# Optimization experiments

Measured on AMD Instinct MI355X. Metric: run time of the kernel, lower is better.

## Reference

```python
import jax, jax.numpy as jnp
import numpy as np
import math

L, B, S, D, H, F, C = 2, 2, 1024, 512, 32, 2048, 1000
EPS_LN = 1e-5

def _grid_coords(batch, seq_len):
    g = math.ceil(math.sqrt(seq_len))
    xs = jnp.linspace(0.0, 1.0, g)
    gx, gy = jnp.meshgrid(xs, xs, indexing='ij')
    pts = jnp.stack([gx.ravel(), gy.ravel()], axis=1)
    reps = math.ceil(seq_len / (g * g))
    pts = jnp.tile(pts, (reps, 1))[:seq_len]
    return jnp.broadcast_to(pts[None], (batch, seq_len, 2)).astype(jnp.float32)

def setup_inputs() -> dict:
    key = jax.random.key(0)
    ks = iter(jax.random.split(key, 16))
    sd = 0.02
    inp = {
        'x': jax.random.normal(next(ks), (B, S, D), jnp.float32),
        'coords': _grid_coords(B, S),
        'Wq': jax.random.normal(next(ks), (L, D, D), jnp.float32) * sd,
        'Wk': jax.random.normal(next(ks), (L, D, D), jnp.float32) * sd,
        'Wv': jax.random.normal(next(ks), (L, D, D), jnp.float32) * sd,
        'rot_w1': jax.random.normal(next(ks), (L, 3, H), jnp.float32) * 0.5,
        'rot_b1': jnp.zeros((L, H), jnp.float32),
        'rot_w2': jax.random.normal(next(ks), (L, H), jnp.float32) * 0.1,
        'rot_b2': jnp.zeros((L,), jnp.float32),
        'trans_w1': jax.random.normal(next(ks), (L, 2, H), jnp.float32) * 0.5,
        'trans_b1': jnp.zeros((L, H), jnp.float32),
        'trans_w2': jax.random.normal(next(ks), (L, H), jnp.float32) * 0.1,
        'trans_b2': jnp.zeros((L,), jnp.float32),
        'refl_w1': jax.random.normal(next(ks), (L, 4, H), jnp.float32) * 0.5,
        'refl_b1': jnp.zeros((L, H), jnp.float32),
        'refl_w2': jax.random.normal(next(ks), (L, H), jnp.float32) * 0.1,
        'refl_b2': jnp.zeros((L,), jnp.float32),
        'ln1_g': jnp.ones((L, D), jnp.float32),
        'ln1_b': jnp.zeros((L, D), jnp.float32),
        'ffn_w1': jax.random.normal(next(ks), (L, D, F), jnp.float32) * sd,
        'ffn_b1': jnp.zeros((L, F), jnp.float32),
        'ffn_w2': jax.random.normal(next(ks), (L, F, D), jnp.float32) * sd,
        'ffn_b2': jnp.zeros((L, D), jnp.float32),
        'ln2_g': jnp.ones((L, D), jnp.float32),
        'ln2_b': jnp.zeros((L, D), jnp.float32),
        'lnf_g': jnp.ones((D,), jnp.float32),
        'lnf_b': jnp.zeros((D,), jnp.float32),
        'fc_w': jax.random.normal(next(ks), (D, C), jnp.float32) * sd,
        'fc_b': jnp.zeros((C,), jnp.float32),
    }
    return inp

def _layernorm(x, g, b):
    mu = x.mean(-1, keepdims=True)
    var = ((x - mu) ** 2).mean(-1, keepdims=True)
    return (x - mu) * jax.lax.rsqrt(var + EPS_LN) * g + b

def _pair_mlp(inp, w1, b1, w2, b2):
    # inp: [B,S,S,f] -> [B,S,S]
    h = jax.nn.relu(jnp.einsum('bijf,fh->bijh', inp, w1) + b1)
    return jnp.einsum('bijh,h->bij', h, w2) + b2

def reference(x, coords, Wq, Wk, Wv, rot_w1, rot_b1, rot_w2, rot_b2,
              trans_w1, trans_b1, trans_w2, trans_b2,
              refl_w1, refl_b1, refl_w2, refl_b2,
              ln1_g, ln1_b, ffn_w1, ffn_b1, ffn_w2, ffn_b2, ln2_g, ln2_b,
              lnf_g, lnf_b, fc_w, fc_b):
    d_model = x.shape[-1]
    scale = math.sqrt(d_model)
    # Pairwise relative geometry (layer-independent): rel = coords_j - coords_i
    rel = coords[:, None, :, :] - coords[:, :, None, :]   # [B,S,S,2]
    dx, dy = rel[..., 0], rel[..., 1]
    dist = jnp.sqrt(dx * dx + dy * dy + 1e-8)
    theta = jnp.arctan2(dy, dx)
    rot_in = jnp.stack([dist, jnp.sin(theta), jnp.cos(theta)], axis=-1)  # [B,S,S,3]
    trans_in = rel                                                       # [B,S,S,2]
    refl_in = jnp.concatenate([rel, -rel], axis=-1)                      # [B,S,S,4]

    n_layers = Wq.shape[0]
    for l in range(n_layers):
        Q = x @ Wq[l]
        K = x @ Wk[l]
        V = x @ Wv[l]
        scores = jnp.einsum('bid,bjd->bij', Q, K) / scale
        scores = scores \
            + _pair_mlp(rot_in, rot_w1[l], rot_b1[l], rot_w2[l], rot_b2[l]) \
            + _pair_mlp(trans_in, trans_w1[l], trans_b1[l], trans_w2[l], trans_b2[l]) \
            + _pair_mlp(refl_in, refl_w1[l], refl_b1[l], refl_w2[l], refl_b2[l])
        attn = jax.nn.softmax(scores, axis=-1)
        attn_out = jnp.einsum('bij,bjd->bid', attn, V)
        x = _layernorm(x + attn_out, ln1_g[l], ln1_b[l])
        ffn = jax.nn.relu(x @ ffn_w1[l] + ffn_b1[l]) @ ffn_w2[l] + ffn_b2[l]
        x = _layernorm(x + ffn, ln2_g[l], ln2_b[l])

    x = _layernorm(x, lnf_g, lnf_b)
    pooled = x.mean(axis=1)          # [B,D]
    return pooled @ fc_w + fc_b      # [B,C]
```

## Files before the change

### kernel.cpp

```cpp
#include <hip/hip_runtime.h>
#include <hip/hip_bf16.h>

using bf16 = __hip_bfloat16;
typedef __attribute__((ext_vector_type(8))) short short8;
typedef __attribute__((ext_vector_type(4))) float f32x4;

constexpr int NLAYER = 2;
constexpr int NB = 2;
constexpr int NS = 1024;
constexpr int ND = 512;
constexpr int NH = 32;
constexpr int NF = 2048;
constexpr int NC = 1000;
constexpr float EPS_LN = 1e-5f;

__device__ inline unsigned short f2bfu(float x) {
    union { bf16 h; unsigned short u; } c;
    c.h = __float2bfloat16(x);
    return c.u;
}

#define GLOAD16(gp, lp) __builtin_amdgcn_global_load_lds( \
    (const __attribute__((address_space(1))) void*)(gp),  \
    (__attribute__((address_space(3))) void*)(lp), 16, 0, 0)

template<int BM, int BN, bool OUTBF, bool RELU, bool SCORES, bool VOUT>
__global__ __launch_bounds__(256) void mfma_gemm(
    const bf16* __restrict__ A, const bf16* __restrict__ B,
    const float* __restrict__ bias, void* __restrict__ Cout,
    const float* __restrict__ table, bf16* __restrict__ vT,
    int K, int lda, int ldb, int ldc,
    long sA, long sB, long sC, float alpha)
{
    const int bz = blockIdx.z;
    A += (long)bz * sA;
    B += (long)bz * sB;
    const int bm = blockIdx.y * BM, bn = blockIdx.x * BN;
    __shared__ bf16 As[2][BM * 32], Bs[2][BN * 32];
    const int tid = threadIdx.x, lane = tid & 63, wv = tid >> 6;
    const int wr = (wv >> 1) * (BM / 2), wc = (wv & 1) * (BN / 2);
    constexpr int FM = BM / 32, FN = BN / 32;
    f32x4 acc[FM][FN] = {};
    const int r_a = tid >> 2;
    const int ko = (tid & 3) * 8;

    auto stage = [&](int buf, int k0) {
        #pragma unroll
        for (int c = 0; c < BM / 64; ++c)
            GLOAD16(A + (long)(bm + r_a + c * 64) * lda + k0 + ko,
                    &As[buf][c * 2048 + wv * 512]);
        #pragma unroll
        for (int c = 0; c < BN / 64; ++c)
            GLOAD16(B + (long)(bn + r_a + c * 64) * ldb + k0 + ko,
                    &Bs[buf][c * 2048 + wv * 512]);
    };

    const int nt = K >> 5;
    stage(0, 0);
    __syncthreads();
    for (int t = 0; t < nt; ++t) {
        const int cur = t & 1;
        if (t + 1 < nt) stage(cur ^ 1, (t + 1) << 5);
        const short8* Asv = (const short8*)As[cur];
        const short8* Bsv = (const short8*)Bs[cur];
        short8 af[FM], bfr[FN];
        #pragma unroll
        for (int m = 0; m < FM; ++m)
            af[m] = Asv[(wr + m * 16 + (lane & 15)) * 4 + (lane >> 4)];
        #pragma unroll
        for (int n = 0; n < FN; ++n)
            bfr[n] = Bsv[(wc + n * 16 + (lane & 15)) * 4 + (lane >> 4)];
        #pragma unroll
        for (int m = 0; m < FM; ++m)
            #pragma unroll
            for (int n = 0; n < FN; ++n)
                acc[m][n] = __builtin_amdgcn_mfma_f32_16x16x32_bf16(
                    af[m], bfr[n], acc[m][n], 0, 0, 0);
        __syncthreads();
    }

    const int er = (lane >> 4) * 4, ec = lane & 15;
    #pragma unroll
    for (int m = 0; m < FM; ++m) {
        #pragma unroll
        for (int n = 0; n < FN; ++n) {
            const int row0 = bm + wr + m * 16 + er;
            const int col  = bn + wc + n * 16 + ec;
            const float bv = bias ? bias[col] : 0.f;
            #pragma unroll
            for (int e = 0; e < 4; ++e) {
                const int row = row0 + e;
                float v = acc[m][n][e];
                if (SCORES) {
                    int di = (col >> 5) - (row >> 5) + 31;
                    int dj = (col & 31) - (row & 31) + 31;
                    v = v * alpha + table[di * 63 + dj];
                } else {
                    v += bv;
                    if (RELU) v = fmaxf(v, 0.f);
                }
                if (OUTBF)
                    ((bf16*)Cout)[bz * sC + (long)row * ldc + col] = __float2bfloat16(v);
                else
                    ((float*)Cout)[bz * sC + (long)row * ldc + col] = v;
                if (VOUT && col >= 2 * ND) {
                    int bb = row >> 10;
                    vT[(long)bb * ND * NS + (long)(col - 2 * ND) * NS + (row & (NS - 1))] =
                        __float2bfloat16(v);
                }
            }
        }
    }
}

__global__ __launch_bounds__(256) void tconv_qkv_kernel(
    const float* __restrict__ Wq, const float* __restrict__ Wk,
    const float* __restrict__ Wv, bf16* __restrict__ dst)
{
    const int z = blockIdx.z;
    const int l = z / 3, wsel = z % 3;
    const float* src = (wsel == 0 ? Wq : wsel == 1 ? Wk : Wv) + (long)l * ND * ND;
    bf16* d = dst + (long)l * 3 * ND * ND + (long)wsel * ND * ND;
    __shared__ float t[32][33];
    const int c0 = blockIdx.x * 32, r0 = blockIdx.y * 32;
    const int lx = threadIdx.x & 31, ly = threadIdx.x >> 5;
    for (int rr = ly; rr < 32; rr += 8)
        t[rr][lx] = src[(long)(r0 + rr) * ND + c0 + lx];
    __syncthreads();
    for (int cc = ly; cc < 32; cc += 8)
        d[(long)(c0 + cc) * ND + r0 + lx] = __float2bfloat16(t[lx][cc]);
}

__global__ __launch_bounds__(256) void tconv_f32_kernel(
    const float* __restrict__ src, bf16* __restrict__ dst,
    int R, int C, long sS, long sD)
{
    src += (long)blockIdx.z * sS;
    dst += (long)blockIdx.z * sD;
    __shared__ float t[32][33];
    const int c0 = blockIdx.x * 32, r0 = blockIdx.y * 32;
    const int lx = threadIdx.x & 31, ly = threadIdx.x >> 5;
    for (int rr = ly; rr < 32; rr += 8)
        t[rr][lx] = src[(long)(r0 + rr) * C + c0 + lx];
    __syncthreads();
    for (int cc = ly; cc < 32; cc += 8)
        dst[(long)(c0 + cc) * R + r0 + lx] = __float2bfloat16(t[lx][cc]);
}

__global__ __launch_bounds__(256) void xcopy_kernel(
    const float* __restrict__ xin, float* __restrict__ xc, bf16* __restrict__ xb)
{
    long i = (long)blockIdx.x * 256 + threadIdx.x;
    float4 v = ((const float4*)xin)[i];
    ((float4*)xc)[i] = v;
    uint2 o;
    o.x = (unsigned)f2bfu(v.x) | ((unsigned)f2bfu(v.y) << 16);
    o.y = (unsigned)f2bfu(v.z) | ((unsigned)f2bfu(v.w) << 16);
    ((uint2*)xb)[i] = o;
}

__global__ __launch_bounds__(256) void bias_table_kernel(
    const float* __restrict__ coords,
    const float* __restrict__ rot_w1, const float* __restrict__ rot_b1,
    const float* __restrict__ rot_w2, const float* __restrict__ rot_b2,
    const float* __restrict__ trans_w1, const float* __restrict__ trans_b1,
    const float* __restrict__ trans_w2, const float* __restrict__ trans_b2,
    const float* __restrict__ refl_w1, const float* __restrict__ refl_b1,
    const float* __restrict__ refl_w2, const float* __restrict__ refl_b2,
    float* __restrict__ table)
{
    int idx = blockIdx.x * 256 + threadIdx.x;
    if (idx >= 63 * 63) return;
    int da = idx / 63 - 31, db = idx % 63 - 31;
    int ai = da < 0 ? -da : 0, bi = db < 0 ? -db : 0;
    int i = ai * 32 + bi, j = (ai + da) * 32 + (bi + db);
    float2 ci = ((const float2*)coords)[i];
    float2 cj = ((const float2*)coords)[j];
    float dx = cj.x - ci.x, dy = cj.y - ci.y;
    float dist = sqrtf(dx * dx + dy * dy + 1e-8f);
    float th = atan2f(dy, dx);
    float sn = sinf(th), cs = cosf(th);

    #pragma unroll
    for (int l = 0; l < NLAYER; ++l) {
        const float* rw1 = rot_w1 + l * 3 * NH;
        const float* rb1 = rot_b1 + l * NH;
        const float* rw2 = rot_w2 + l * NH;
        const float* tw1 = trans_w1 + l * 2 * NH;
        const float* tb1 = trans_b1 + l * NH;
        const float* tw2 = trans_w2 + l * NH;
        const float* fw1 = refl_w1 + l * 4 * NH;
        const float* fb1 = refl_b1 + l * NH;
        const float* fw2 = refl_w2 + l * NH;
        float acc = rot_b2[l] + trans_b2[l] + refl_b2[l];
        #pragma unroll 8
        for (int h = 0; h < NH; ++h) {
            float hr = fmaxf(dist * rw1[h] + sn * rw1[NH + h] + cs * rw1[2 * NH + h] + rb1[h], 0.f);
            acc += hr * rw2[h];
            float ht = fmaxf(dx * tw1[h] + dy * tw1[NH + h] + tb1[h], 0.f);
            acc += ht * tw2[h];
            float hf = fmaxf(dx * fw1[h] + dy * fw1[NH + h] - dx * fw1[2 * NH + h] - dy * fw1[3 * NH + h] + fb1[h], 0.f);
            acc += hf * fw2[h];
        }
        table[l * 3969 + idx] = acc;
    }
}

__global__ __launch_bounds__(256) void init_tail_kernel(
    const float* __restrict__ fc_b, float* __restrict__ out, float* __restrict__ pooled)
{
    int i = blockIdx.x * 256 + threadIdx.x;
    if (i < NB * NC) out[i] = fc_b[i % NC];
    int j = i - NB * NC;
    if (j >= 0 && j < NB * ND) pooled[j] = 0.f;
}

__global__ __launch_bounds__(256) void softmax_kernel(
    const float* __restrict__ sc, bf16* __restrict__ P)
{
    const float* p = sc + (long)blockIdx.x * NS;
    const int tid = threadIdx.x;
    float4 v = ((const float4*)p)[tid];
    float m = fmaxf(fmaxf(v.x, v.y), fmaxf(v.z, v.w));
    #pragma unroll
    for (int off = 32; off; off >>= 1) m = fmaxf(m, __shfl_xor(m, off));
    __shared__ float red[4], red2[4];
    int wid = tid >> 6;
    if ((tid & 63) == 0) red[wid] = m;
    __syncthreads();
    m = fmaxf(fmaxf(red[0], red[1]), fmaxf(red[2], red[3]));
    v.x = __expf(v.x - m); v.y = __expf(v.y - m);
    v.z = __expf(v.z - m); v.w = __expf(v.w - m);
    float s = v.x + v.y + v.z + v.w;
    #pragma unroll
    for (int off = 32; off; off >>= 1) s += __shfl_xor(s, off);
    if ((tid & 63) == 0) red2[wid] = s;
    __syncthreads();
    s = red2[0] + red2[1] + red2[2] + red2[3];
    float inv = 1.f / s;
    uint2 o;
    o.x = (unsigned)f2bfu(v.x * inv) | ((unsigned)f2bfu(v.y * inv) << 16);
    o.y = (unsigned)f2bfu(v.z * inv) | ((unsigned)f2bfu(v.w * inv) << 16);
    ((uint2*)(P + (long)blockIdx.x * NS))[tid] = o;
}

__global__ __launch_bounds__(256) void add_ln_kernel(
    const float* __restrict__ x, const float* __restrict__ res,
    const float* __restrict__ g, const float* __restrict__ bt,
    float* __restrict__ out, bf16* __restrict__ outb)
{
    long row = blockIdx.x;
    const int tid = threadIdx.x;
    float2 xv = ((const float2*)(x + row * ND))[tid];
    if (res) {
        float2 rv = ((const float2*)(res + row * ND))[tid];
        xv.x += rv.x; xv.y += rv.y;
    }
    float s = xv.x + xv.y;
    float ss = xv.x * xv.x + xv.y * xv.y;
    #pragma unroll
    for (int off = 32; off; off >>= 1) {
        s += __shfl_xor(s, off);
        ss += __shfl_xor(ss, off);
    }
    __shared__ float rs[4], rss[4];
    int wid = tid >> 6;
    if ((tid & 63) == 0) { rs[wid] = s; rss[wid] = ss; }
    __syncthreads();
    s = rs[0] + rs[1] + rs[2] + rs[3];
    ss = rss[0] + rss[1] + rss[2] + rss[3];
    float mu = s * (1.f / ND);
    float var = ss * (1.f / ND) - mu * mu;
    float inv = rsqrtf(var + EPS_LN);
    float2 gv = ((const float2*)g)[tid];
    float2 bv = ((const float2*)bt)[tid];
    float2 o;
    o.x = (xv.x - mu) * inv * gv.x + bv.x;
    o.y = (xv.y - mu) * inv * gv.y + bv.y;
    ((float2*)(out + row * ND))[tid] = o;
    if (outb)
        ((unsigned int*)(outb + row * ND))[tid] =
            (unsigned)f2bfu(o.x) | ((unsigned)f2bfu(o.y) << 16);
}

__global__ __launch_bounds__(256) void pool_kernel(
    const float* __restrict__ x, float* __restrict__ pooled)
{
    const int tid = threadIdx.x;
    const long row0 = (long)blockIdx.x * 16;
    const int b = (int)(row0 >> 10);
    float ax = 0.f, ay = 0.f, az = 0.f, aw = 0.f;
    #pragma unroll
    for (int it = 0; it < 8; ++it) {
        long r = row0 + it * 2 + (tid >> 7);
        float4 v = ((const float4*)(x + r * ND))[tid & 127];
        ax += v.x; ay += v.y; az += v.z; aw += v.w;
    }
    __shared__ float red[256][4];
    red[tid][0] = ax; red[tid][1] = ay; red[tid][2] = az; red[tid][3] = aw;
    __syncthreads();
    if (tid < 128) {
        int d = tid * 4;
        atomicAdd(&pooled[b * ND + d + 0], (red[tid][0] + red[tid + 128][0]) * (1.f / NS));
        atomicAdd(&pooled[b * ND + d + 1], (red[tid][1] + red[tid + 128][1]) * (1.f / NS));
        atomicAdd(&pooled[b * ND + d + 2], (red[tid][2] + red[tid + 128][2]) * (1.f / NS));
        atomicAdd(&pooled[b * ND + d + 3], (red[tid][3] + red[tid + 128][3]) * (1.f / NS));
    }
}

__global__ __launch_bounds__(256) void fc_kernel(
    const float* __restrict__ pooled, const float* __restrict__ w,
    float* __restrict__ out)
{
    const int lane = threadIdx.x & 63, dg = threadIdx.x >> 6;
    const int c = blockIdx.x * 64 + lane;
    const int b = blockIdx.y;
    const int d0 = blockIdx.z * 64 + dg * 16;
    const bool ok = (c < NC);
    const float* p = pooled + b * ND;
    float acc = 0.f;
    #pragma unroll
    for (int d = 0; d < 16; ++d)
        acc += p[d0 + d] * (ok ? w[(long)(d0 + d) * NC + c] : 0.f);
    __shared__ float red[4][64];
    red[dg][lane] = acc;
    __syncthreads();
    if (dg == 0 && ok)
        atomicAdd(&out[(long)b * NC + c],
                  red[0][lane] + red[1][lane] + red[2][lane] + red[3][lane]);
}

extern "C" void kernel_launch(void* const* d_in, const int* in_sizes, int n_in,
                              void* d_out, int out_size, void* d_ws, size_t ws_size,
                              hipStream_t stream)
{
    const float* x_in   = (const float*)d_in[0];
    const float* coords = (const float*)d_in[1];
    const float* Wq     = (const float*)d_in[2];
    const float* Wk     = (const float*)d_in[3];
    const float* Wv     = (const float*)d_in[4];
    const float* rot_w1 = (const float*)d_in[5];
    const float* rot_b1 = (const float*)d_in[6];
    const float* rot_w2 = (const float*)d_in[7];
    const float* rot_b2 = (const float*)d_in[8];
    const float* trans_w1 = (const float*)d_in[9];
    const float* trans_b1 = (const float*)d_in[10];
    const float* trans_w2 = (const float*)d_in[11];
    const float* trans_b2 = (const float*)d_in[12];
    const float* refl_w1 = (const float*)d_in[13];
    const float* refl_b1 = (const float*)d_in[14];
    const float* refl_w2 = (const float*)d_in[15];
    const float* refl_b2 = (const float*)d_in[16];
    const float* ln1_g = (const float*)d_in[17];
    const float* ln1_b = (const float*)d_in[18];
    const float* ffn_w1 = (const float*)d_in[19];
    const float* ffn_b1 = (const float*)d_in[20];
    const float* ffn_w2 = (const float*)d_in[21];
    const float* ffn_b2 = (const float*)d_in[22];
    const float* ln2_g = (const float*)d_in[23];
    const float* ln2_b = (const float*)d_in[24];
    const float* lnf_g = (const float*)d_in[25];
    const float* lnf_b = (const float*)d_in[26];
    const float* fc_w = (const float*)d_in[27];
    const float* fc_b = (const float*)d_in[28];
    float* out = (float*)d_out;

    const long XSZ = (long)NB * NS * ND;
    const long SSZ = (long)NB * NS * NS;

    char* wp = (char*)d_ws;
    auto alloc = [&](long bytes) -> char* {
        char* p = wp; wp += (bytes + 255) & ~(long)255; return p;
    };
    float* x_cur  = (float*)alloc(XSZ * 4);
    bf16*  xb     = (bf16*)alloc(XSZ * 2);
    bf16*  qkv    = (bf16*)alloc((long)NB * NS * 1536 * 2);
    bf16*  vT     = (bf16*)alloc((long)NB * ND * NS * 2);
    float* sc     = (float*)alloc(SSZ * 4);
    bf16*  pb     = (bf16*)alloc(SSZ * 2);
    float* ao     = (float*)alloc(XSZ * 4);
    bf16*  hfb    = (bf16*)alloc((long)NB * NS * NF * 2);
    bf16*  wqkvT  = (bf16*)alloc((long)NLAYER * 3 * ND * ND * 2);
    bf16*  w1T    = (bf16*)alloc((long)NLAYER * NF * ND * 2);
    bf16*  w2T    = (bf16*)alloc((long)NLAYER * ND * NF * 2);
    float* table  = (float*)alloc((long)NLAYER * 3969 * 4);
    float* pooled = (float*)alloc((long)NB * ND * 4);

    const float inv_scale = 1.0f / sqrtf((float)ND);
    const long QKVLD = 1536;

    tconv_qkv_kernel<<<dim3(16, 16, 3 * NLAYER), 256, 0, stream>>>(Wq, Wk, Wv, wqkvT);
    tconv_f32_kernel<<<dim3(64, 16, NLAYER), 256, 0, stream>>>(
        ffn_w1, w1T, ND, NF, (long)ND * NF, (long)NF * ND);
    tconv_f32_kernel<<<dim3(16, 64, NLAYER), 256, 0, stream>>>(
        ffn_w2, w2T, NF, ND, (long)NF * ND, (long)ND * NF);

    xcopy_kernel<<<dim3((int)(XSZ / 1024)), 256, 0, stream>>>(x_in, x_cur, xb);

    bias_table_kernel<<<dim3(16), 256, 0, stream>>>(
        coords, rot_w1, rot_b1, rot_w2, rot_b2,
        trans_w1, trans_b1, trans_w2, trans_b2,
        refl_w1, refl_b1, refl_w2, refl_b2, table);

    init_tail_kernel<<<dim3(12), 256, 0, stream>>>(fc_b, out, pooled);

    for (int l = 0; l < NLAYER; ++l) {
        mfma_gemm<128, 128, true, false, false, true>
            <<<dim3(1536 / 128, (NB * NS) / 128, 1), 256, 0, stream>>>(
            xb, wqkvT + (long)l * 3 * ND * ND, nullptr, qkv, nullptr, vT,
            ND, ND, ND, QKVLD, 0, 0, 0, 0.f);

        mfma_gemm<128, 128, false, false, true, false>
            <<<dim3(NS / 128, NS / 128, NB), 256, 0, stream>>>(
            qkv, qkv + ND, nullptr, sc, table + (long)l * 3969, nullptr,
            ND, QKVLD, QKVLD, NS, (long)NS * QKVLD, (long)NS * QKVLD,
            (long)NS * NS, inv_scale);

        softmax_kernel<<<dim3(NB * NS), 256, 0, stream>>>(sc, pb);

        mfma_gemm<128, 64, false, false, false, false>
            <<<dim3(ND / 64, NS / 128, NB), 256, 0, stream>>>(
            pb, vT, nullptr, ao, nullptr, nullptr,
            NS, NS, NS, ND, (long)NS * NS, (long)ND * NS, (long)NS * ND, 0.f);

        add_ln_kernel<<<dim3(NB * NS), 256, 0, stream>>>(
            x_cur, ao, ln1_g + (long)l * ND, ln1_b + (long)l * ND, x_cur, xb);

        mfma_gemm<128, 128, true, true, false, false>
            <<<dim3(NF / 128, (NB * NS) / 128, 1), 256, 0, stream>>>(
            xb, w1T + (long)l * NF * ND, ffn_b1 + (long)l * NF, hfb, nullptr, nullptr,
            ND, ND, ND, NF, 0, 0, 0, 0.f);

        mfma_gemm<128, 64, false, false, false, false>
            <<<dim3(ND / 64, (NB * NS) / 128, 1), 256, 0, stream>>>(
            hfb, w2T + (long)l * ND * NF, ffn_b2 + (long)l * ND, ao, nullptr, nullptr,
            NF, NF, NF, ND, 0, 0, 0, 0.f);

        add_ln_kernel<<<dim3(NB * NS), 256, 0, stream>>>(
            x_cur, ao, ln2_g + (long)l * ND, ln2_b + (long)l * ND, x_cur, xb);
    }

    add_ln_kernel<<<dim3(NB * NS), 256, 0, stream>>>(
        x_cur, nullptr, lnf_g, lnf_b, x_cur, nullptr);

    pool_kernel<<<dim3((NB * NS) / 16), 256, 0, stream>>>(x_cur, pooled);

    fc_kernel<<<dim3((NC + 63) / 64, NB, ND / 64), 256, 0, stream>>>(pooled, fc_w, out);
}
```

Measured before the change: 388.4 us.

## Use 8-wave GEMM blocks and merge setup kernels into fewer launches

The MFMA GEMM now runs with 512 threads (8 waves) and a configurable wave grid, so each wave computes a smaller sub-tile. The staging loop is rewritten to distribute 16-row chunks across waves. The PV and FFN2 GEMMs switch from 128x64 tiles to 64x128 tiles. The weight transposes are merged into one launch, and the x copy, bias table and output init into another, to cut launch overhead. The trade-off is fewer accumulator registers per wave for more waves per block. More threads can also share each LDS tile, which changes barrier cost.

Measured after the change: 384.3 us. About the same (-1.0%).

```diff
diff --git a/kernel.cpp b/kernel.cpp
--- a/kernel.cpp
+++ b/kernel.cpp
@@ -24,8 +24,8 @@
     (const __attribute__((address_space(1))) void*)(gp),  \
     (__attribute__((address_space(3))) void*)(lp), 16, 0, 0)
 
-template<int BM, int BN, bool OUTBF, bool RELU, bool SCORES, bool VOUT>
-__global__ __launch_bounds__(256) void mfma_gemm(
+template<int BM, int BN, int WR, int WC, bool OUTBF, bool RELU, bool SCORES, bool VOUT>
+__global__ __launch_bounds__(512) void mfma_gemm(
     const bf16* __restrict__ A, const bf16* __restrict__ B,
     const float* __restrict__ bias, void* __restrict__ Cout,
     const float* __restrict__ table, bf16* __restrict__ vT,
@@ -38,21 +38,26 @@
     const int bm = blockIdx.y * BM, bn = blockIdx.x * BN;
     __shared__ bf16 As[2][BM * 32], Bs[2][BN * 32];
     const int tid = threadIdx.x, lane = tid & 63, wv = tid >> 6;
-    const int wr = (wv >> 1) * (BM / 2), wc = (wv & 1) * (BN / 2);
-    constexpr int FM = BM / 32, FN = BN / 32;
+    constexpr int WM = BM / WR, WN = BN / WC;
+    constexpr int FM = WM / 16, FN = WN / 16;
+    const int wr = (wv / WC) * WM, wc = (wv % WC) * WN;
     f32x4 acc[FM][FN] = {};
-    const int r_a = tid >> 2;
-    const int ko = (tid & 3) * 8;
+    const int ko = (lane & 3) * 8;
+    constexpr int ACH = BM / 16;
+    constexpr int BCH = BN / 16;
+    constexpr int NCH = ACH + BCH;
 
     auto stage = [&](int buf, int k0) {
-        #pragma unroll
-        for (int c = 0; c < BM / 64; ++c)
-            GLOAD16(A + (long)(bm + r_a + c * 64) * lda + k0 + ko,
-                    &As[buf][c * 2048 + wv * 512]);
-        #pragma unroll
-        for (int c = 0; c < BN / 64; ++c)
-            GLOAD16(B + (long)(bn + r_a + c * 64) * ldb + k0 + ko,
-                    &Bs[buf][c * 2048 + wv * 512]);
+        for (int c = wv; c < NCH; c += 8) {
+            if (c < ACH) {
+                int r = c * 16 + (lane >> 2);
+                GLOAD16(A + (long)(bm + r) * lda + k0 + ko, &As[buf][c * 512]);
+            } else {
+                int cc = c - ACH;
+                int r = cc * 16 + (lane >> 2);
+                GLOAD16(B + (long)(bn + r) * ldb + k0 + ko, &Bs[buf][cc * 512]);
+            }
+        }
     };
 
     const int nt = K >> 5;
@@ -113,32 +118,32 @@
     }
 }
 
-__global__ __launch_bounds__(256) void tconv_qkv_kernel(
+__global__ __launch_bounds__(256) void wtrans_kernel(
     const float* __restrict__ Wq, const float* __restrict__ Wk,
-    const float* __restrict__ Wv, bf16* __restrict__ dst)
-{
-    const int z = blockIdx.z;
-    const int l = z / 3, wsel = z % 3;
-    const float* src = (wsel == 0 ? Wq : wsel == 1 ? Wk : Wv) + (long)l * ND * ND;
-    bf16* d = dst + (long)l * 3 * ND * ND + (long)wsel * ND * ND;
+    const float* __restrict__ Wv, const float* __restrict__ ffn_w1,
+    const float* __restrict__ ffn_w2, bf16* __restrict__ wqkvT,
+    bf16* __restrict__ w1T, bf16* __restrict__ w2T)
+{
+    const int s = blockIdx.x;
+    const float* src; bf16* dst; int R, C, r0, c0;
+    if (s < 1536) {
+        int z = s >> 8, rem = s & 255;
+        int l = z / 3, wsel = z % 3;
+        src = (wsel == 0 ? Wq : wsel == 1 ? Wk : Wv) + (long)l * ND * ND;
+        dst = wqkvT + (long)l * 3 * ND * ND + (long)wsel * ND * ND;
+        R = ND; C = ND; c0 = (rem & 15) * 32; r0 = (rem >> 4) * 32;
+    } else if (s < 3584) {
+        int t = s - 1536, l = t >> 10, rem = t & 1023;
+        src = ffn_w1 + (long)l * ND * NF;
+        dst = w1T + (long)l * NF * ND;
+        R = ND; C = NF; c0 = (rem & 63) * 32; r0 = (rem >> 6) * 32;
+    } else {
+        int t = s - 3584, l = t >> 10, rem = t & 1023;
+        src = ffn_w2 + (long)l * NF * ND;
+        dst = w2T + (long)l * ND * NF;
+        R = NF; C = ND; c0 = (rem & 15) * 32; r0 = (rem >> 4) * 32;
+    }
     __shared__ float t[32][33];
-    const int c0 = blockIdx.x * 32, r0 = blockIdx.y * 32;
-    const int lx = threadIdx.x & 31, ly = threadIdx.x >> 5;
-    for (int rr = ly; rr < 32; rr += 8)
-        t[rr][lx] = src[(long)(r0 + rr) * ND + c0 + lx];
-    __syncthreads();
-    for (int cc = ly; cc < 32; cc += 8)
-        d[(long)(c0 + cc) * ND + r0 + lx] = __float2bfloat16(t[lx][cc]);
-}
-
-__global__ __launch_bounds__(256) void tconv_f32_kernel(
-    const float* __restrict__ src, bf16* __restrict__ dst,
-    int R, int C, long sS, long sD)
-{
-    src += (long)blockIdx.z * sS;
-    dst += (long)blockIdx.z * sD;
-    __shared__ float t[32][33];
-    const int c0 = blockIdx.x * 32, r0 = blockIdx.y * 32;
     const int lx = threadIdx.x & 31, ly = threadIdx.x >> 5;
     for (int rr = ly; rr < 32; rr += 8)
         t[rr][lx] = src[(long)(r0 + rr) * C + c0 + lx];
@@ -147,19 +152,8 @@
         dst[(long)(c0 + cc) * R + r0 + lx] = __float2bfloat16(t[lx][cc]);
 }
 
-__global__ __launch_bounds__(256) void xcopy_kernel(
-    const float* __restrict__ xin, float* __restrict__ xc, bf16* __restrict__ xb)
-{
-    long i = (long)blockIdx.x * 256 + threadIdx.x;
-    float4 v = ((const float4*)xin)[i];
-    ((float4*)xc)[i] = v;
-    uint2 o;
-    o.x = (unsigned)f2bfu(v.x) | ((unsigned)f2bfu(v.y) << 16);
-    o.y = (unsigned)f2bfu(v.z) | ((unsigned)f2bfu(v.w) << 16);
-    ((uint2*)xb)[i] = o;
-}
-
-__global__ __launch_bounds__(256) void bias_table_kernel(
+__global__ __launch_bounds__(256) void prep_kernel(
+    const float* __restrict__ xin, float* __restrict__ xc, bf16* __restrict__ xb,
     const float* __restrict__ coords,
     const float* __restrict__ rot_w1, const float* __restrict__ rot_b1,
     const float* __restrict__ rot_w2, const float* __restrict__ rot_b2,
@@ -167,52 +161,64 @@
     const float* __restrict__ trans_w2, const float* __restrict__ trans_b2,
     const float* __restrict__ refl_w1, const float* __restrict__ refl_b1,
     const float* __restrict__ refl_w2, const float* __restrict__ refl_b2,
-    float* __restrict__ table)
-{
-    int idx = blockIdx.x * 256 + threadIdx.x;
-    if (idx >= 63 * 63) return;
-    int da = idx / 63 - 31, db = idx % 63 - 31;
-    int ai = da < 0 ? -da : 0, bi = db < 0 ? -db : 0;
-    int i = ai * 32 + bi, j = (ai + da) * 32 + (bi + db);
-    float2 ci = ((const float2*)coords)[i];
-    float2 cj = ((const float2*)coords)[j];
-    float dx = cj.x - ci.x, dy = cj.y - ci.y;
-    float dist = sqrtf(dx * dx + dy * dy + 1e-8f);
-    float th = atan2f(dy, dx);
-    float sn = sinf(th), cs = cosf(th);
-
-    #pragma unroll
-    for (int l = 0; l < NLAYER; ++l) {
-        const float* rw1 = rot_w1 + l * 3 * NH;
-        const float* rb1 = rot_b1 + l * NH;
-        const float* rw2 = rot_w2 + l * NH;
-        const float* tw1 = trans_w1 + l * 2 * NH;
-        const float* tb1 = trans_b1 + l * NH;
-        const float* tw2 = trans_w2 + l * NH;
-        const float* fw1 = refl_w1 + l * 4 * NH;
-        const float* fb1 = refl_b1 + l * NH;
-        const float* fw2 = refl_w2 + l * NH;
-        float acc = rot_b2[l] + trans_b2[l] + refl_b2[l];
-        #pragma unroll 8
-        for (int h = 0; h < NH; ++h) {
-            float hr = fmaxf(dist * rw1[h] + sn * rw1[NH + h] + cs * rw1[2 * NH + h] + rb1[h], 0.f);
-            acc += hr * rw2[h];
-            float ht = fmaxf(dx * tw1[h] + dy * tw1[NH + h] + tb1[h], 0.f);
-            acc += ht * tw2[h];
-            float hf = fmaxf(dx * fw1[h] + dy * fw1[NH + h] - dx * fw1[2 * NH + h] - dy * fw1[3 * NH + h] + fb1[h], 0.f);
-            acc += hf * fw2[h];
+    float* __restrict__ table,
+    const float* __restrict__ fc_b, float* __restrict__ out,
+    float* __restrict__ pooled)
+{
+    const int blk = blockIdx.x, tid = threadIdx.x;
+    if (blk < 1024) {
+        long i = (long)blk * 256 + tid;
+        float4 v = ((const float4*)xin)[i];
+        ((float4*)xc)[i] = v;
+        uint2 o;
+        o.x = (unsigned)f2bfu(v.x) | ((unsigned)f2bfu(v.y) << 16);
+        o.y = (unsigned)f2bfu(v.z) | ((unsigned)f2bfu(v.w) << 16);
+        ((uint2*)xb)[i] = o;
+        return;
+    }
+    if (blk < 1040) {
+        int idx = (blk - 1024) * 256 + tid;
+        if (idx >= 63 * 63) return;
+        int da = idx / 63 - 31, db = idx % 63 - 31;
+        int ai = da < 0 ? -da : 0, bi = db < 0 ? -db : 0;
+        int i = ai * 32 + bi, j = (ai + da) * 32 + (bi + db);
+        float2 ci = ((const float2*)coords)[i];
+        float2 cj = ((const float2*)coords)[j];
+        float dx = cj.x - ci.x, dy = cj.y - ci.y;
+        float dist = sqrtf(dx * dx + dy * dy + 1e-8f);
+        float th = atan2f(dy, dx);
+        float sn = sinf(th), cs = cosf(th);
+        #pragma unroll
+        for (int l = 0; l < NLAYER; ++l) {
+            const float* rw1 = rot_w1 + l * 3 * NH;
+            const float* rb1 = rot_b1 + l * NH;
+            const float* rw2 = rot_w2 + l * NH;
+            const float* tw1 = trans_w1 + l * 2 * NH;
+            const float* tb1 = trans_b1 + l * NH;
+            const float* tw2 = trans_w2 + l * NH;
+            const float* fw1 = refl_w1 + l * 4 * NH;
+            const float* fb1 = refl_b1 + l * NH;
+            const float* fw2 = refl_w2 + l * NH;
+            float acc = rot_b2[l] + trans_b2[l] + refl_b2[l];
+            #pragma unroll 8
+            for (int h = 0; h < NH; ++h) {
+                float hr = fmaxf(dist * rw1[h] + sn * rw1[NH + h] + cs * rw1[2 * NH + h] + rb1[h], 0.f);
+                acc += hr * rw2[h];
+                float ht = fmaxf(dx * tw1[h] + dy * tw1[NH + h] + tb1[h], 0.f);
+                acc += ht * tw2[h];
+                float hf = fmaxf(dx * fw1[h] + dy * fw1[NH + h] - dx * fw1[2 * NH + h] - dy * fw1[3 * NH + h] + fb1[h], 0.f);
+                acc += hf * fw2[h];
+            }
+            table[l * 3969 + idx] = acc;
         }
-        table[l * 3969 + idx] = acc;
-    }
-}
-
-__global__ __launch_bounds__(256) void init_tail_kernel(
-    const float* __restrict__ fc_b, float* __restrict__ out, float* __restrict__ pooled)
-{
-    int i = blockIdx.x * 256 + threadIdx.x;
-    if (i < NB * NC) out[i] = fc_b[i % NC];
-    int j = i - NB * NC;
-    if (j >= 0 && j < NB * ND) pooled[j] = 0.f;
+        return;
+    }
+    {
+        int i = (blk - 1040) * 256 + tid;
+        if (i < NB * NC) out[i] = fc_b[i % NC];
+        int j = i - NB * NC;
+        if (j >= 0 && j < NB * ND) pooled[j] = 0.f;
+    }
 }
 
 __global__ __launch_bounds__(256) void softmax_kernel(
@@ -389,50 +395,45 @@
     const float inv_scale = 1.0f / sqrtf((float)ND);
     const long QKVLD = 1536;
 
-    tconv_qkv_kernel<<<dim3(16, 16, 3 * NLAYER), 256, 0, stream>>>(Wq, Wk, Wv, wqkvT);
-    tconv_f32_kernel<<<dim3(64, 16, NLAYER), 256, 0, stream>>>(
-        ffn_w1, w1T, ND, NF, (long)ND * NF, (long)NF * ND);
-    tconv_f32_kernel<<<dim3(16, 64, NLAYER), 256, 0, stream>>>(
-        ffn_w2, w2T, NF, ND, (long)NF * ND, (long)ND * NF);
-
-    xcopy_kernel<<<dim3((int)(XSZ / 1024)), 256, 0, stream>>>(x_in, x_cur, xb);
-
-    bias_table_kernel<<<dim3(16), 256, 0, stream>>>(
-        coords, rot_w1, rot_b1, rot_w2, rot_b2,
+    wtrans_kernel<<<dim3(5632), 256, 0, stream>>>(
+        Wq, Wk, Wv, ffn_w1, ffn_w2, wqkvT, w1T, w2T);
+
+    prep_kernel<<<dim3(1052), 256, 0, stream>>>(
+        x_in, x_cur, xb, coords,
+        rot_w1, rot_b1, rot_w2, rot_b2,
         trans_w1, trans_b1, trans_w2, trans_b2,
-        refl_w1, refl_b1, refl_w2, refl_b2, table);
-
-    init_tail_kernel<<<dim3(12), 256, 0, stream>>>(fc_b, out, pooled);
+        refl_w1, refl_b1, refl_w2, refl_b2, table,
+        fc_b, out, pooled);
 
     for (int l = 0; l < NLAYER; ++l) {
-        mfma_gemm<128, 128, true, false, false, true>
-            <<<dim3(1536 / 128, (NB * NS) / 128, 1), 256, 0, stream>>>(
+        mfma_gemm<128, 128, 4, 2, true, false, false, true>
+            <<<dim3(1536 / 128, (NB * NS) / 128, 1), 512, 0, stream>>>(
             xb, wqkvT + (long)l * 3 * ND * ND, nullptr, qkv, nullptr, vT,
             ND, ND, ND, QKVLD, 0, 0, 0, 0.f);
 
-        mfma_gemm<128, 128, false, false, true, false>
-            <<<dim3(NS / 128, NS / 128, NB), 256, 0, stream>>>(
+        mfma_gemm<128, 128, 4, 2, false, false, true, false>
+            <<<dim3(NS / 128, NS / 128, NB), 512, 0, stream>>>(
             qkv, qkv + ND, nullptr, sc, table + (long)l * 3969, nullptr,
             ND, QKVLD, QKVLD, NS, (long)NS * QKVLD, (long)NS * QKVLD,
             (long)NS * NS, inv_scale);
 
         softmax_kernel<<<dim3(NB * NS), 256, 0, stream>>>(sc, pb);
 
-        mfma_gemm<128, 64, false, false, false, false>
-            <<<dim3(ND / 64, NS / 128, NB), 256, 0, stream>>>(
+        mfma_gemm<64, 128, 2, 4, false, false, false, false>
+            <<<dim3(ND / 128, NS / 64, NB), 512, 0, stream>>>(
             pb, vT, nullptr, ao, nullptr, nullptr,
             NS, NS, NS, ND, (long)NS * NS, (long)ND * NS, (long)NS * ND, 0.f);
 
         add_ln_kernel<<<dim3(NB * NS), 256, 0, stream>>>(
             x_cur, ao, ln1_g + (long)l * ND, ln1_b + (long)l * ND, x_cur, xb);
 
-        mfma_gemm<128, 128, true, true, false, false>
-            <<<dim3(NF / 128, (NB * NS) / 128, 1), 256, 0, stream>>>(
+        mfma_gemm<128, 128, 4, 2, true, true, false, false>
+            <<<dim3(NF / 128, (NB * NS) / 128, 1), 512, 0, stream>>>(
             xb, w1T + (long)l * NF * ND, ffn_b1 + (long)l * NF, hfb, nullptr, nullptr,
             ND, ND, ND, NF, 0, 0, 0, 0.f);
 
-        mfma_gemm<128, 64, false, false, false, false>
-            <<<dim3(ND / 64, (NB * NS) / 128, 1), 256, 0, stream>>>(
+        mfma_gemm<64, 128, 2, 4, false, false, false, false>
+            <<<dim3(ND / 128, (NB * NS) / 64, 1), 512, 0, stream>>>(
             hfb, w2T + (long)l * ND * NF, ffn_b2 + (long)l * ND, ao, nullptr, nullptr,
             NF, NF, NF, ND, 0, 0, 0, 0.f);
 
```
